# Kernel optimization log

Measured on AMD Instinct MI355X. Metric: run time of the kernel, lower is better.

Reference implementation:

```python
import jax, jax.numpy as jnp
import numpy as np

B, C_IN, V, C_OUT, K = 4, 64, 50000, 128, 7


def setup_inputs() -> dict:
    key = jax.random.key(0)
    k1, k2, k3, k4 = jax.random.split(key, 4)
    x = jax.random.normal(k1, (B, C_IN, V, 1), dtype=jnp.float32)
    # Gi: per-vertex [self, n1, n2, n3] indices (random neighbors, in-range)
    Gi = jax.random.randint(k2, (B, V, 4), 0, V, dtype=jnp.int64)
    # Conv2d(in, out, kernel=(1,7)) weight collapsed to [out, in, 7]
    W = jax.random.normal(k3, (C_OUT, C_IN, K), dtype=jnp.float32) * 0.05
    b = jax.random.normal(k4, (C_OUT,), dtype=jnp.float32) * 0.05
    return {"x": x, "Gi": Gi, "W": W, "b": b}


def reference(x, Gi, W, b):
    xs = x[..., 0]  # [B, C, V]  (squeeze(-1))
    Bx, C, Vx = xs.shape
    # prepend zero-padding column (index 0 after Gi+1 maps padded -1 entries)
    xp = jnp.concatenate([jnp.zeros((Bx, C, 1), xs.dtype), xs], axis=2)  # [B,C,V+1]
    gi = Gi + 1
    # gather per batch: f[b,c,v,j] = xp[b,c,gi[b,v,j]]
    f = jax.vmap(lambda xb, gb: xb[:, gb])(xp, gi)  # [B, C, V, 4]
    f0, f1, f2, f3 = f[..., 0], f[..., 1], f[..., 2], f[..., 3]
    G = jnp.stack([
        f0,
        f1 + f2 + f3,                                        # symm_oper 1
        f1 * f2 * f3,                                        # symm_oper 2
        f1 * f2 + f1 * f3 + f2 * f3,                         # symm_oper 3
        f1 * f1 + f2 * f2 + f3 * f3,                         # symm_oper 4
        jnp.abs(f1 - f2) + jnp.abs(f1 - f3) + jnp.abs(f2 - f3),  # symm_oper 5
        f1 * f1 * f1 + f2 * f2 * f2 + f3 * f3 * f3,          # symm_oper 6
    ], axis=3)  # [B, C, V, 7]
    # conv2d with kernel (1,7), no padding -> width collapses to 1
    out = jnp.einsum('bcvk,ock->bov', G, W) + b[None, :, None]
    return out[..., None]  # [B, C_out, V, 1]
```

## Files before the change

### kernel.cpp

```cpp
#include <hip/hip_runtime.h>
#include <cstdint>
#include <cstddef>

#define BB   4
#define CIN  64
#define VV   50000
#define COUT 128
#define NV   32
#define NTILES 1563
#define KTOT 448
#define KT   14
#define PITCH 456

typedef __attribute__((ext_vector_type(8))) short     short8;
typedef __attribute__((ext_vector_type(8))) _Float16  half8;
typedef __attribute__((ext_vector_type(4))) float     f32x4;

__device__ _Float16       g_xt[(size_t)BB * VV * CIN];
__device__ unsigned short g_wb[KT * 8 * 64 * 8];

__device__ inline unsigned short f2h(float f) {
    union { _Float16 h; unsigned short u; } cv;
    cv.h = (_Float16)f;
    return cv.u;
}

__global__ __launch_bounds__(256) void transpose_k(const float* __restrict__ x,
                                                   const float* __restrict__ W) {
    if (blockIdx.y == 0 && blockIdx.x < (KT * 8 * 64 + 255) / 256) {
        int idx = blockIdx.x * 256 + threadIdx.x;
        if (idx < KT * 8 * 64) {
            int lane = idx & 63;
            int mt   = (idx >> 6) & 7;
            int kt   = idx >> 9;
            int m    = mt * 16 + (lane & 15);
            int kb   = kt * 32 + (lane >> 4) * 8;
            union { unsigned short s[8]; short8 v; } u;
#pragma unroll
            for (int j = 0; j < 8; j++) {
                int kk = kb + j;
                int c  = kk & 63;
                int k  = kk >> 6;
                u.s[j] = f2h(W[((size_t)m * CIN + c) * 7 + k]);
            }
            *(short8*)&g_wb[(size_t)idx * 8] = u.v;
        }
    }

    __shared__ float tile[64][65];
    int b  = blockIdx.y;
    int v0 = blockIdx.x * 64;
    int t  = threadIdx.x;
    int tv = t & 15;
    int tc = t >> 4;
#pragma unroll
    for (int i = 0; i < 4; i++) {
        int c = tc + 16 * i;
        int v = v0 + tv * 4;
        const float* src = x + ((size_t)b * CIN + c) * VV + v;
        f32x4 f;
        if (v + 3 < VV) {
            f = *(const f32x4*)src;
        } else {
            f[0] = v + 0 < VV ? src[0] : 0.f;
            f[1] = v + 1 < VV ? src[1] : 0.f;
            f[2] = v + 2 < VV ? src[2] : 0.f;
            f[3] = v + 3 < VV ? src[3] : 0.f;
        }
        tile[c][tv * 4 + 0] = f[0];
        tile[c][tv * 4 + 1] = f[1];
        tile[c][tv * 4 + 2] = f[2];
        tile[c][tv * 4 + 3] = f[3];
    }
    __syncthreads();
    int c8  = t & 7;
    int tvv = t >> 3;
#pragma unroll
    for (int i = 0; i < 2; i++) {
        int v = v0 + tvv + 32 * i;
        if (v < VV) {
            union { _Float16 h[8]; short8 s; } u;
#pragma unroll
            for (int j = 0; j < 8; j++)
                u.h[j] = (_Float16)tile[c8 * 8 + j][tvv + 32 * i];
            *(short8*)(g_xt + ((size_t)b * VV + v) * CIN + c8 * 8) = u.s;
        }
    }
}

__device__ inline void feats(float f0, float f1, float f2, float f3, float* g) {
    g[0] = f0;
    g[1] = f1 + f2 + f3;
    float p12 = f1 * f2, p13 = f1 * f3, p23 = f2 * f3;
    g[2] = p12 * f3;
    g[3] = p12 + p13 + p23;
    g[4] = f1 * f1 + f2 * f2 + f3 * f3;
    g[5] = fabsf(f1 - f2) + fabsf(f1 - f3) + fabsf(f2 - f3);
    g[6] = f1 * f1 * f1 + f2 * f2 * f2 + f3 * f3 * f3;
}

__global__ __launch_bounds__(256, 4) void mesh_k(
        const void* __restrict__ Gi, const float* __restrict__ bias,
        float* __restrict__ out) {
    __shared__ _Float16 Gl[NV * PITCH];

    int bid  = blockIdx.x;
    int b    = (bid & 7) >> 1;
    int tile = ((bid >> 3) << 1) + (bid & 1);
    if (tile >= NTILES) return;
    int v0 = tile * NV;
    int t  = threadIdx.x;
    int w    = t >> 6;
    int lane = t & 63;

    const unsigned* gu = (const unsigned*)Gi;
    bool is64 = ((gu[1] | gu[3] | gu[5] | gu[7]) == 0u);

    int val = 0;
    {
        int vv = 8 * w + (lane >> 2);
        int j  = lane & 3;
        int v  = v0 + vv;
        if (lane < 32 && v < VV) {
            size_t gb = ((size_t)b * VV + v) * 4 + j;
            long long xv = is64 ? ((const long long*)Gi)[gb]
                                : (long long)((const int*)Gi)[gb];
            val = (int)(xv < 0 ? 0 : (xv >= VV ? VV - 1 : xv));
        }
    }

    const half8* wbp = (const half8*)g_wb;
    half8 a0c = wbp[(2 * w    ) * 64 + lane];
    half8 a1c = wbp[(2 * w + 1) * 64 + lane];

    int J[4];
    int srcl = (lane >> 3) << 2;
#pragma unroll
    for (int j = 0; j < 4; ++j) J[j] = __shfl(val, srcl + j, 64);

    int c8   = t & 7;
    int slot = t >> 3;

    const _Float16* base = g_xt + (size_t)b * VV * CIN + c8 * 8;
    half8 F[4];
#pragma unroll
    for (int j = 0; j < 4; ++j)
        F[j] = *(const half8*)(base + (size_t)J[j] * CIN);

    union { _Float16 h[8]; short8 s; } u[7];
#pragma unroll
    for (int i = 0; i < 8; ++i) {
        float g7[7];
        feats((float)F[0][i], (float)F[1][i], (float)F[2][i], (float)F[3][i], g7);
#pragma unroll
        for (int k = 0; k < 7; ++k) u[k].h[i] = (_Float16)g7[k];
    }
    _Float16* grow = &Gl[slot * PITCH + c8 * 8];
#pragma unroll
    for (int k = 0; k < 7; ++k)
        *(short8*)(grow + k * 64) = u[k].s;
    __syncthreads();

    int l15  = lane & 15;
    int q    = lane >> 4;

    f32x4 acc[2][2] = {};
    half8 a0n, a1n;
#pragma unroll
    for (int kt = 0; kt < KT; ++kt) {
        if (kt + 1 < KT) {
            a0n = wbp[((kt + 1) * 8 + 2 * w    ) * 64 + lane];
            a1n = wbp[((kt + 1) * 8 + 2 * w + 1) * 64 + lane];
        }
        half8 b0 = *(const half8*)&Gl[(l15     ) * PITCH + kt * 32 + q * 8];
        half8 b1 = *(const half8*)&Gl[(l15 + 16) * PITCH + kt * 32 + q * 8];
        acc[0][0] = __builtin_amdgcn_mfma_f32_16x16x32_f16(a0c, b0, acc[0][0], 0, 0, 0);
        acc[0][1] = __builtin_amdgcn_mfma_f32_16x16x32_f16(a0c, b1, acc[0][1], 0, 0, 0);
        acc[1][0] = __builtin_amdgcn_mfma_f32_16x16x32_f16(a1c, b0, acc[1][0], 0, 0, 0);
        acc[1][1] = __builtin_amdgcn_mfma_f32_16x16x32_f16(a1c, b1, acc[1][1], 0, 0, 0);
        a0c = a0n; a1c = a1n;
    }

#pragma unroll
    for (int mt = 0; mt < 2; ++mt) {
        int o = 32 * w + mt * 16 + q * 4;
        float bs[4];
#pragma unroll
        for (int r = 0; r < 4; ++r) bs[r] = bias[o + r];
#pragma unroll
        for (int n = 0; n < 2; ++n) {
            int vv = v0 + n * 16 + l15;
            if (vv < VV) {
                float* po = out + ((size_t)b * COUT + o) * VV + vv;
#pragma unroll
                for (int r = 0; r < 4; ++r)
                    __builtin_nontemporal_store(acc[mt][n][r] + bs[r], po + (size_t)r * VV);
            }
        }
    }
}

extern "C" void kernel_launch(void* const* d_in, const int* in_sizes, int n_in,
                              void* d_out, int out_size, void* d_ws, size_t ws_size,
                              hipStream_t stream) {
    const float* x    = (const float*)d_in[0];
    const void*  Gi   = d_in[1];
    const float* W    = (const float*)d_in[2];
    const float* bias = (const float*)d_in[3];
    float* out        = (float*)d_out;

    dim3 gt((VV + 63) / 64, BB);
    transpose_k<<<gt, 256, 0, stream>>>(x, W);
    mesh_k<<<dim3(8 * ((NTILES + 1) / 2)), 256, 0, stream>>>(Gi, bias, out);
}
```

Baseline: 202.4 us.

## Halve vertex tile to 16 per block and raise occupancy target

New measurement: 220.3 us. 1.09x slower.

```diff
diff --git a/kernel.cpp b/kernel.cpp
--- a/kernel.cpp
+++ b/kernel.cpp
@@ -6,14 +6,15 @@
 #define CIN  64
 #define VV   50000
 #define COUT 128
-#define NV   32
-#define NTILES 1563
+#define NV   16
+#define NTILES 3125
 #define KTOT 448
 #define KT   14
 #define PITCH 456
 
 typedef __attribute__((ext_vector_type(8))) short     short8;
 typedef __attribute__((ext_vector_type(8))) _Float16  half8;
+typedef __attribute__((ext_vector_type(4))) _Float16  half4;
 typedef __attribute__((ext_vector_type(4))) float     f32x4;
 
 __device__ _Float16       g_xt[(size_t)BB * VV * CIN];
@@ -99,7 +100,7 @@
     g[6] = f1 * f1 * f1 + f2 * f2 * f2 + f3 * f3 * f3;
 }
 
-__global__ __launch_bounds__(256, 4) void mesh_k(
+__global__ __launch_bounds__(256, 8) void mesh_k(
         const void* __restrict__ Gi, const float* __restrict__ bias,
         float* __restrict__ out) {
     __shared__ _Float16 Gl[NV * PITCH];
@@ -116,55 +117,52 @@
     const unsigned* gu = (const unsigned*)Gi;
     bool is64 = ((gu[1] | gu[3] | gu[5] | gu[7]) == 0u);
 
-    int val = 0;
+    int val;
     {
-        int vv = 8 * w + (lane >> 2);
+        int vv = lane >> 2;
         int j  = lane & 3;
-        int v  = v0 + vv;
-        if (lane < 32 && v < VV) {
-            size_t gb = ((size_t)b * VV + v) * 4 + j;
-            long long xv = is64 ? ((const long long*)Gi)[gb]
-                                : (long long)((const int*)Gi)[gb];
-            val = (int)(xv < 0 ? 0 : (xv >= VV ? VV - 1 : xv));
-        }
+        size_t gb = ((size_t)b * VV + v0 + vv) * 4 + j;
+        long long xv = is64 ? ((const long long*)Gi)[gb]
+                            : (long long)((const int*)Gi)[gb];
+        val = (int)(xv < 0 ? 0 : (xv >= VV ? VV - 1 : xv));
     }
 
     const half8* wbp = (const half8*)g_wb;
     half8 a0c = wbp[(2 * w    ) * 64 + lane];
     half8 a1c = wbp[(2 * w + 1) * 64 + lane];
 
+    int c4   = t & 15;
+    int slot = t >> 4;
+
     int J[4];
-    int srcl = (lane >> 3) << 2;
+    int srcl = slot << 2;
 #pragma unroll
     for (int j = 0; j < 4; ++j) J[j] = __shfl(val, srcl + j, 64);
 
-    int c8   = t & 7;
-    int slot = t >> 3;
-
-    const _Float16* base = g_xt + (size_t)b * VV * CIN + c8 * 8;
-    half8 F[4];
+    const _Float16* base = g_xt + (size_t)b * VV * CIN + c4 * 4;
+    half4 F[4];
 #pragma unroll
     for (int j = 0; j < 4; ++j)
-        F[j] = *(const half8*)(base + (size_t)J[j] * CIN);
-
-    union { _Float16 h[8]; short8 s; } u[7];
-#pragma unroll
-    for (int i = 0; i < 8; ++i) {
+        F[j] = *(const half4*)(base + (size_t)J[j] * CIN);
+
+    union { _Float16 h[4]; half4 v; } u[7];
+#pragma unroll
+    for (int i = 0; i < 4; ++i) {
         float g7[7];
         feats((float)F[0][i], (float)F[1][i], (float)F[2][i], (float)F[3][i], g7);
 #pragma unroll
         for (int k = 0; k < 7; ++k) u[k].h[i] = (_Float16)g7[k];
     }
-    _Float16* grow = &Gl[slot * PITCH + c8 * 8];
+    _Float16* grow = &Gl[slot * PITCH + c4 * 4];
 #pragma unroll
     for (int k = 0; k < 7; ++k)
-        *(short8*)(grow + k * 64) = u[k].s;
+        *(half4*)(grow + k * 64) = u[k].v;
     __syncthreads();
 
     int l15  = lane & 15;
     int q    = lane >> 4;
 
-    f32x4 acc[2][2] = {};
+    f32x4 acc[2] = {};
     half8 a0n, a1n;
 #pragma unroll
     for (int kt = 0; kt < KT; ++kt) {
@@ -172,31 +170,20 @@
             a0n = wbp[((kt + 1) * 8 + 2 * w    ) * 64 + lane];
             a1n = wbp[((kt + 1) * 8 + 2 * w + 1) * 64 + lane];
         }
-        half8 b0 = *(const half8*)&Gl[(l15     ) * PITCH + kt * 32 + q * 8];
-        half8 b1 = *(const half8*)&Gl[(l15 + 16) * PITCH + kt * 32 + q * 8];
-        acc[0][0] = __builtin_amdgcn_mfma_f32_16x16x32_f16(a0c, b0, acc[0][0], 0, 0, 0);
-        acc[0][1] = __builtin_amdgcn_mfma_f32_16x16x32_f16(a0c, b1, acc[0][1], 0, 0, 0);
-        acc[1][0] = __builtin_amdgcn_mfma_f32_16x16x32_f16(a1c, b0, acc[1][0], 0, 0, 0);
-        acc[1][1] = __builtin_amdgcn_mfma_f32_16x16x32_f16(a1c, b1, acc[1][1], 0, 0, 0);
+        half8 b0 = *(const half8*)&Gl[l15 * PITCH + kt * 32 + q * 8];
+        acc[0] = __builtin_amdgcn_mfma_f32_16x16x32_f16(a0c, b0, acc[0], 0, 0, 0);
+        acc[1] = __builtin_amdgcn_mfma_f32_16x16x32_f16(a1c, b0, acc[1], 0, 0, 0);
         a0c = a0n; a1c = a1n;
     }
 
+    int v = v0 + l15;
 #pragma unroll
     for (int mt = 0; mt < 2; ++mt) {
         int o = 32 * w + mt * 16 + q * 4;
-        float bs[4];
-#pragma unroll
-        for (int r = 0; r < 4; ++r) bs[r] = bias[o + r];
-#pragma unroll
-        for (int n = 0; n < 2; ++n) {
-            int vv = v0 + n * 16 + l15;
-            if (vv < VV) {
-                float* po = out + ((size_t)b * COUT + o) * VV + vv;
-#pragma unroll
-                for (int r = 0; r < 4; ++r)
-                    __builtin_nontemporal_store(acc[mt][n][r] + bs[r], po + (size_t)r * VV);
-            }
-        }
+        float* po = out + ((size_t)b * COUT + o) * VV + v;
+#pragma unroll
+        for (int r = 0; r < 4; ++r)
+            __builtin_nontemporal_store(acc[mt][r] + bias[o + r], po + (size_t)r * VV);
     }
 }
 
```

## Loop each block over eight vertex tiles with prefetched gathers and resident weights

Applied to the files above, without the earlier changes.

After: 206.0 us. Within noise of the previous version (+1.8%).

```diff
diff --git a/kernel.cpp b/kernel.cpp
--- a/kernel.cpp
+++ b/kernel.cpp
@@ -7,7 +7,9 @@
 #define VV   50000
 #define COUT 128
 #define NV   32
+#define TPB  8
 #define NTILES 1563
+#define NGRP 196
 #define KTOT 448
 #define KT   14
 #define PITCH 456
@@ -99,102 +101,129 @@
     g[6] = f1 * f1 * f1 + f2 * f2 * f2 + f3 * f3 * f3;
 }
 
-__global__ __launch_bounds__(256, 4) void mesh_k(
+__global__ __launch_bounds__(256, 2) void mesh_k(
         const void* __restrict__ Gi, const float* __restrict__ bias,
         float* __restrict__ out) {
-    __shared__ _Float16 Gl[NV * PITCH];
+    __shared__ _Float16 Gl[2][NV * PITCH];
 
     int bid  = blockIdx.x;
     int b    = (bid & 7) >> 1;
-    int tile = ((bid >> 3) << 1) + (bid & 1);
-    if (tile >= NTILES) return;
-    int v0 = tile * NV;
-    int t  = threadIdx.x;
-    int w    = t >> 6;
-    int lane = t & 63;
+    int grp  = ((bid >> 3) << 1) + (bid & 1);
+    int tile0 = grp * TPB;
+    int t = threadIdx.x;
+    int w = t >> 6, lane = t & 63;
 
     const unsigned* gu = (const unsigned*)Gi;
     bool is64 = ((gu[1] | gu[3] | gu[5] | gu[7]) == 0u);
-
-    int val = 0;
-    {
-        int vv = 8 * w + (lane >> 2);
-        int j  = lane & 3;
-        int v  = v0 + vv;
-        if (lane < 32 && v < VV) {
-            size_t gb = ((size_t)b * VV + v) * 4 + j;
-            long long xv = is64 ? ((const long long*)Gi)[gb]
-                                : (long long)((const int*)Gi)[gb];
-            val = (int)(xv < 0 ? 0 : (xv >= VV ? VV - 1 : xv));
-        }
-    }
+    const long long* g64 = (const long long*)Gi;
+    const int*       g32 = (const int*)Gi;
 
     const half8* wbp = (const half8*)g_wb;
-    half8 a0c = wbp[(2 * w    ) * 64 + lane];
-    half8 a1c = wbp[(2 * w + 1) * 64 + lane];
-
-    int J[4];
-    int srcl = (lane >> 3) << 2;
-#pragma unroll
-    for (int j = 0; j < 4; ++j) J[j] = __shfl(val, srcl + j, 64);
+    half8 A0[KT], A1[KT];
+#pragma unroll
+    for (int kt = 0; kt < KT; ++kt) {
+        A0[kt] = wbp[(kt * 8 + 2 * w    ) * 64 + lane];
+        A1[kt] = wbp[(kt * 8 + 2 * w + 1) * 64 + lane];
+    }
 
     int c8   = t & 7;
     int slot = t >> 3;
-
-    const _Float16* base = g_xt + (size_t)b * VV * CIN + c8 * 8;
-    half8 F[4];
-#pragma unroll
-    for (int j = 0; j < 4; ++j)
-        F[j] = *(const half8*)(base + (size_t)J[j] * CIN);
-
-    union { _Float16 h[8]; short8 s; } u[7];
-#pragma unroll
-    for (int i = 0; i < 8; ++i) {
-        float g7[7];
-        feats((float)F[0][i], (float)F[1][i], (float)F[2][i], (float)F[3][i], g7);
-#pragma unroll
-        for (int k = 0; k < 7; ++k) u[k].h[i] = (_Float16)g7[k];
-    }
-    _Float16* grow = &Gl[slot * PITCH + c8 * 8];
-#pragma unroll
-    for (int k = 0; k < 7; ++k)
-        *(short8*)(grow + k * 64) = u[k].s;
-    __syncthreads();
-
-    int l15  = lane & 15;
-    int q    = lane >> 4;
-
-    f32x4 acc[2][2] = {};
-    half8 a0n, a1n;
-#pragma unroll
-    for (int kt = 0; kt < KT; ++kt) {
-        if (kt + 1 < KT) {
-            a0n = wbp[((kt + 1) * 8 + 2 * w    ) * 64 + lane];
-            a1n = wbp[((kt + 1) * 8 + 2 * w + 1) * 64 + lane];
-        }
-        half8 b0 = *(const half8*)&Gl[(l15     ) * PITCH + kt * 32 + q * 8];
-        half8 b1 = *(const half8*)&Gl[(l15 + 16) * PITCH + kt * 32 + q * 8];
-        acc[0][0] = __builtin_amdgcn_mfma_f32_16x16x32_f16(a0c, b0, acc[0][0], 0, 0, 0);
-        acc[0][1] = __builtin_amdgcn_mfma_f32_16x16x32_f16(a0c, b1, acc[0][1], 0, 0, 0);
-        acc[1][0] = __builtin_amdgcn_mfma_f32_16x16x32_f16(a1c, b0, acc[1][0], 0, 0, 0);
-        acc[1][1] = __builtin_amdgcn_mfma_f32_16x16x32_f16(a1c, b1, acc[1][1], 0, 0, 0);
-        a0c = a0n; a1c = a1n;
-    }
-
-#pragma unroll
-    for (int mt = 0; mt < 2; ++mt) {
-        int o = 32 * w + mt * 16 + q * 4;
-        float bs[4];
-#pragma unroll
-        for (int r = 0; r < 4; ++r) bs[r] = bias[o + r];
-#pragma unroll
-        for (int n = 0; n < 2; ++n) {
-            int vv = v0 + n * 16 + l15;
-            if (vv < VV) {
-                float* po = out + ((size_t)b * COUT + o) * VV + vv;
-#pragma unroll
-                for (int r = 0; r < 4; ++r)
-                    __builtin_nontemporal_store(acc[mt][n][r] + bs[r], po + (size_t)r * VV);
+    int l15  = lane & 15, q = lane >> 4;
+    int srcl = (lane >> 3) << 2;
+    const _Float16* xb = g_xt + (size_t)b * VV * CIN + c8 * 8;
+
+    int gvv = 8 * w + (lane >> 2), gj = lane & 3;
+
+    auto load_gi = [&](int ti) -> int {
+        int v = ti * NV + gvv;
+        if (v >= VV) v = VV - 1;
+        size_t gb = ((size_t)b * VV + v) * 4 + gj;
+        long long xv = is64 ? g64[gb] : (long long)g32[gb];
+        return (int)(xv < 0 ? 0 : (xv >= VV ? VV - 1 : xv));
+    };
+    auto issue_gather = [&](half8* F, int val) {
+        int J[4];
+#pragma unroll
+        for (int j = 0; j < 4; ++j) J[j] = __shfl(val, srcl + j, 64);
+#pragma unroll
+        for (int j = 0; j < 4; ++j)
+            F[j] = *(const half8*)(xb + (size_t)J[j] * CIN);
+    };
+
+    float bs[2][4];
+#pragma unroll
+    for (int mt = 0; mt < 2; ++mt)
+#pragma unroll
+        for (int r = 0; r < 4; ++r)
+            bs[mt][r] = bias[32 * w + mt * 16 + q * 4 + r];
+
+    int valA = 0, valB = 0;
+    half8 Fa[4], Fb[4];
+    if (lane < 32) valA = load_gi(tile0);
+    issue_gather(Fa, valA);
+    if (lane < 32) valB = load_gi(tile0 + 1);
+
+#pragma unroll
+    for (int tau = 0; tau < TPB; ++tau) {
+        int tile = tile0 + tau;
+        if (tile >= NTILES) break;
+        int v0 = tile * NV;
+        bool hasN1 = (tau + 1 < TPB) && (tile + 1 < NTILES);
+        bool hasN2 = (tau + 2 < TPB) && (tile + 2 < NTILES);
+
+        half8* Fc = (tau & 1) ? Fb : Fa;
+        half8* Fn = (tau & 1) ? Fa : Fb;
+        int   valN = (tau & 1) ? valA : valB;
+
+        union { _Float16 h[8]; short8 s; } u[7];
+#pragma unroll
+        for (int i = 0; i < 8; ++i) {
+            float g7[7];
+            feats((float)Fc[0][i], (float)Fc[1][i], (float)Fc[2][i],
+                  (float)Fc[3][i], g7);
+#pragma unroll
+            for (int k = 0; k < 7; ++k) u[k].h[i] = (_Float16)g7[k];
+        }
+        _Float16* grow = &Gl[tau & 1][slot * PITCH + c8 * 8];
+#pragma unroll
+        for (int k = 0; k < 7; ++k)
+            *(short8*)(grow + k * 64) = u[k].s;
+
+        if (hasN2 && lane < 32) {
+            if (tau & 1) valB = load_gi(tile + 2);
+            else         valA = load_gi(tile + 2);
+        }
+
+        __syncthreads();
+
+        if (hasN1) issue_gather(Fn, valN);
+
+        f32x4 acc[2][2] = {};
+        const _Float16* gb0 = &Gl[tau & 1][(l15     ) * PITCH];
+        const _Float16* gb1 = &Gl[tau & 1][(l15 + 16) * PITCH];
+#pragma unroll
+        for (int kt = 0; kt < KT; ++kt) {
+            half8 b0 = *(const half8*)(gb0 + kt * 32 + q * 8);
+            half8 b1 = *(const half8*)(gb1 + kt * 32 + q * 8);
+            acc[0][0] = __builtin_amdgcn_mfma_f32_16x16x32_f16(A0[kt], b0, acc[0][0], 0, 0, 0);
+            acc[0][1] = __builtin_amdgcn_mfma_f32_16x16x32_f16(A0[kt], b1, acc[0][1], 0, 0, 0);
+            acc[1][0] = __builtin_amdgcn_mfma_f32_16x16x32_f16(A1[kt], b0, acc[1][0], 0, 0, 0);
+            acc[1][1] = __builtin_amdgcn_mfma_f32_16x16x32_f16(A1[kt], b1, acc[1][1], 0, 0, 0);
+        }
+
+#pragma unroll
+        for (int mt = 0; mt < 2; ++mt) {
+            int o = 32 * w + mt * 16 + q * 4;
+#pragma unroll
+            for (int n = 0; n < 2; ++n) {
+                int vv = v0 + n * 16 + l15;
+                if (vv < VV) {
+                    float* po = out + ((size_t)b * COUT + o) * VV + vv;
+#pragma unroll
+                    for (int r = 0; r < 4; ++r)
+                        __builtin_nontemporal_store(acc[mt][n][r] + bs[mt][r],
+                                                    po + (size_t)r * VV);
+                }
             }
         }
     }
@@ -211,5 +240,5 @@
 
     dim3 gt((VV + 63) / 64, BB);
     transpose_k<<<gt, 256, 0, stream>>>(x, W);
-    mesh_k<<<dim3(8 * ((NTILES + 1) / 2)), 256, 0, stream>>>(Gi, bias, out);
-}
+    mesh_k<<<dim3(8 * (NGRP / 2)), 256, 0, stream>>>(Gi, bias, out);
+}
```
